# Performance work log

Measured on AMD Instinct MI355X. Metric: run time of the kernel, lower is better.

## Reference

```python
import jax, jax.numpy as jnp
import numpy as np


def _chamfer_min_sqdist(a, b):
    # a: [N,3], b: [M,3] -> for each point in a, min squared distance to b. [N]
    # ||a||^2 + ||b||^2 - 2 a.b^T ; clamp tiny negatives from cancellation.
    a2 = jnp.sum(a * a, axis=-1)            # [N]
    b2 = jnp.sum(b * b, axis=-1)            # [M]
    cross = a @ b.T                          # [N,M] GEMM, K=3
    d = a2[:, None] + b2[None, :] - 2.0 * cross
    return jnp.maximum(jnp.min(d, axis=1), 0.0)


def setup_inputs() -> dict:
    key = jax.random.key(0)
    k1, k2 = jax.random.split(key)
    N = 16384
    state_x = jax.random.normal(k1, (N, 3), dtype=jnp.float32)
    target = jax.random.normal(k2, (N, 3), dtype=jnp.float32)
    return {"state_x": state_x, "target": target}


def reference(state_x, target):
    # dist1: target -> nearest in state_x ; dist2: state_x -> nearest in target
    dist1 = _chamfer_min_sqdist(target, state_x)   # [N]
    dist2 = _chamfer_min_sqdist(state_x, target)   # [N]
    loss = (jnp.mean(jnp.sqrt(dist1)) + jnp.mean(jnp.sqrt(dist2))) * 0.5
    return loss * 10.0
```

## Files before the change

kernel.cpp:

```cpp
#include <hip/hip_runtime.h>
#include <math.h>


typedef __attribute__((ext_vector_type(8)))  short bf16x8;
typedef __attribute__((ext_vector_type(16))) float f32x16;

#define S_SLICES 4

__device__ __forceinline__ unsigned enc_f32(float f) {
    int b = __float_as_int(f);
    return (b >= 0) ? ((unsigned)b | 0x80000000u) : ~(unsigned)b;
}
__device__ __forceinline__ float dec_f32(unsigned k) {
    int b = (k & 0x80000000u) ? (int)(k & 0x7FFFFFFFu) : ~(int)k;
    return __int_as_float(b);
}

__device__ __forceinline__ unsigned short f2bf(float v) {
    unsigned u = __float_as_uint(v);
    u += 0x7FFFu + ((u >> 16) & 1u);
    return (unsigned short)(u >> 16);
}
__device__ __forceinline__ float bf2f(unsigned short b) {
    unsigned u = ((unsigned)b) << 16;
    return __uint_as_float(u);
}
__device__ __forceinline__ unsigned pk2(unsigned short lo, unsigned short hi) {
    return (unsigned)lo | ((unsigned)hi << 16);
}

__device__ __forceinline__ f32x16 mfma_v(bf16x8 a, bf16x8 b, f32x16 c) {
    f32x16 d;
    asm("v_mfma_f32_32x32x16_bf16 %0, %1, %2, %3"
        : "=&v"(d) : "v"(a), "v"(b), "v"(c));
    return d;
}

__global__ __launch_bounds__(256) void chamfer_prep(
    const float* __restrict__ state_x, const float* __restrict__ target,
    uint4* __restrict__ AfragS, uint4* __restrict__ AfragT,
    uint4* __restrict__ BfragS, uint4* __restrict__ BfragT,
    unsigned* __restrict__ mins_u, float* __restrict__ out, int N)
{
    const int p = blockIdx.x * 256 + threadIdx.x;
    const float* src = (p < N) ? state_x : target;
    const int i = (p < N) ? p : p - N;

    const float x = src[3*i+0], y = src[3*i+1], z = src[3*i+2];
    const float n2 = fmaf(x, x, fmaf(y, y, z * z));

    const unsigned short hx = f2bf(x), hy = f2bf(y), hz = f2bf(z);
    const unsigned short lx = f2bf(x - bf2f(hx));
    const unsigned short ly = f2bf(y - bf2f(hy));
    const unsigned short lz = f2bf(z - bf2f(hz));
    const unsigned short mhx = f2bf(-2.0f*x), mhy = f2bf(-2.0f*y), mhz = f2bf(-2.0f*z);
    const unsigned short mlx = f2bf(-2.0f*x - bf2f(mhx));
    const unsigned short mly = f2bf(-2.0f*y - bf2f(mhy));
    const unsigned short mlz = f2bf(-2.0f*z - bf2f(mhz));
    const unsigned short hn = f2bf(n2);
    const unsigned short ln = f2bf(n2 - bf2f(hn));
    const unsigned short ONE = 0x3F80;

    uint4 A0 = make_uint4(pk2(mhx,mhy), pk2(mhz,mlx), pk2(mly,mlz), pk2(mhx,mhy));
    uint4 A1 = make_uint4(pk2(mhz,mlx), pk2(mly,mlz), pk2(hn,ln),   pk2(ONE,ONE));
    uint4 B0 = make_uint4(pk2(hx,hy), pk2(hz,hx), pk2(hy,hz), pk2(lx,ly));
    uint4 B1 = make_uint4(pk2(lz,lx), pk2(ly,lz), pk2(ONE,ONE), pk2(hn,ln));

    uint4* Aarr = (p < N) ? AfragS : AfragT;
    uint4* Barr = (p < N) ? BfragS : BfragT;
    Aarr[2*i+0] = A0;  Aarr[2*i+1] = A1;

    const int bbase = (i >> 6) * 128 + ((i >> 5) & 1) * 64 + (i & 31);
    Barr[bbase +  0] = B0;
    Barr[bbase + 32] = B1;

    mins_u[p] = 0xFFFFFFFFu;
    if (p == 0) *out = 0.0f;
}

__global__ __launch_bounds__(256) void chamfer_main(
    const bf16x8* __restrict__ AfragS, const bf16x8* __restrict__ AfragT,
    const bf16x8* __restrict__ BfragS, const bf16x8* __restrict__ BfragT,
    unsigned* __restrict__ mins_u, int N, int S)
{
    const int tid  = threadIdx.x;
    const int lane = tid & 63;
    const int l31  = lane & 31;
    const int half = lane >> 5;
    const int w    = tid >> 6;

    const int bs = blockIdx.x / S;
    const int s  = blockIdx.x % S;
    const int qblk = bs * 256;

    const bf16x8* afr;
    const bf16x8* bfr;
    if (qblk < N) { afr = AfragT + (size_t)qblk * 2;       bfr = BfragS; }
    else          { afr = AfragS + (size_t)(qblk - N) * 2; bfr = BfragT; }

    const int CS = N / S;
    const int NCHUNK = CS / 1024;

    __shared__ uint4 ldsB[2048];

    const int r0 = w * 64;
    const bf16x8 av0 = afr[(r0 +      l31) * 2 + half];
    const bf16x8 av1 = afr[(r0 + 32 + l31) * 2 + half];

    const int boff = half * 32 + l31;

    f32x16 racc0, racc1, zc;
    #pragma unroll
    for (int i = 0; i < 16; ++i) { racc0[i] = 3.0e38f; racc1[i] = 3.0e38f; zc[i] = 0.0f; }

    for (int chunk = 0; chunk < NCHUNK; ++chunk) {
        {
            const uint4* src = (const uint4*)bfr
                             + ((size_t)s * CS + (size_t)chunk * 1024) * 2;
            #pragma unroll
            for (int j = 0; j < 8; ++j)
                ldsB[tid + j * 256] = src[tid + j * 256];
        }
        __syncthreads();
        const bf16x8* lb = (const bf16x8*)ldsB;

        #pragma unroll 2
        for (int it = 0; it < 16; ++it) {
            const bf16x8 b0 = lb[it * 128 + boff];
            const bf16x8 b1 = lb[it * 128 + 64 + boff];
            f32x16 a0 = mfma_v(av0, b0, zc);
            f32x16 a1 = mfma_v(av0, b1, zc);
            f32x16 a2 = mfma_v(av1, b0, zc);
            f32x16 a3 = mfma_v(av1, b1, zc);
            __builtin_amdgcn_sched_barrier(0);
            asm volatile("s_nop 7");
            __builtin_amdgcn_sched_barrier(0);
            #pragma unroll
            for (int i = 0; i < 16; ++i)
                racc0[i] = fminf(fminf(racc0[i], a0[i]), a1[i]);
            #pragma unroll
            for (int i = 0; i < 16; ++i)
                racc1[i] = fminf(fminf(racc1[i], a2[i]), a3[i]);
        }
        __syncthreads();
    }

    float* lf = (float*)ldsB;
    const int cg = l31 >> 2, cl = l31 & 3;
    #pragma unroll
    for (int i = 0; i < 16; ++i) {
        const int row0 = (i & 3) + 8 * (i >> 2) + 4 * half;
        const int row1 = row0 + 32;
        lf[w * 2048 + row0 * 32 + ((cg ^ (row0 & 7)) << 2) + cl] = racc0[i];
        lf[w * 2048 + row1 * 32 + ((cg ^ (row1 & 7)) << 2) + cl] = racc1[i];
    }
    __syncthreads();
    {
        const int r = tid & 63, wr = tid >> 6;
        const float4* rowp = (const float4*)(lf + wr * 2048 + r * 32);
        float m0 = 3.0e38f, m1 = 3.0e38f;
        #pragma unroll
        for (int g = 0; g < 8; g += 2) {
            const float4 v0 = rowp[g ^ (r & 7)];
            const float4 v1 = rowp[(g + 1) ^ (r & 7)];
            m0 = fminf(fminf(m0, v0.x), fminf(v0.y, v0.z));
            m0 = fminf(m0, v0.w);
            m1 = fminf(fminf(m1, v1.x), fminf(v1.y, v1.z));
            m1 = fminf(m1, v1.w);
        }
        atomicMin(&mins_u[qblk + wr * 64 + r], enc_f32(fminf(m0, m1)));
    }
}

__global__ __launch_bounds__(256) void chamfer_finish(
    const unsigned* __restrict__ mins_u, float* __restrict__ out, int N)
{
    const int tid = threadIdx.x;
    const int qi = blockIdx.x * 256 + tid;

    float v = sqrtf(fmaxf(dec_f32(mins_u[qi]), 0.0f));

    for (int off = 32; off > 0; off >>= 1) v += __shfl_down(v, off, 64);
    __shared__ float wsum[4];
    if ((tid & 63) == 0) wsum[tid >> 6] = v;
    __syncthreads();
    if (tid == 0) {
        const float bsum = wsum[0] + wsum[1] + wsum[2] + wsum[3];
        atomicAdd(out, bsum * 5.0f / (float)N);
    }
}

extern "C" void kernel_launch(void* const* d_in, const int* in_sizes, int n_in,
                              void* d_out, int out_size, void* d_ws, size_t ws_size,
                              hipStream_t stream)
{
    const float* state_x = (const float*)d_in[0];
    const float* target  = (const float*)d_in[1];
    float* out = (float*)d_out;

    const int N = in_sizes[0] / 3;
    const int twoN = 2 * N;

    int S = S_SLICES;
    while (S > 1 && (N % (S * 1024)) != 0) S >>= 1;

    char* wsb = (char*)d_ws;
    unsigned* mins_u = (unsigned*)wsb;
    uint4* AfragS = (uint4*)(wsb + (size_t)twoN * 4);
    uint4* AfragT = (uint4*)(wsb + (size_t)twoN * 4 + (size_t)N * 32);
    uint4* BfragS = (uint4*)(wsb + (size_t)twoN * 4 + (size_t)N * 64);
    uint4* BfragT = (uint4*)(wsb + (size_t)twoN * 4 + (size_t)N * 96);

    chamfer_prep<<<twoN / 256, 256, 0, stream>>>(
        state_x, target, AfragS, AfragT, BfragS, BfragT, mins_u, out, N);

    const int rowBlocks = twoN / 256;
    chamfer_main<<<rowBlocks * S, 256, 0, stream>>>(
        (const bf16x8*)AfragS, (const bf16x8*)AfragT,
        (const bf16x8*)BfragS, (const bf16x8*)BfragT, mins_u, N, S);

    chamfer_finish<<<twoN / 256, 256, 0, stream>>>(mins_u, out, N);
}
```

Before: 81.90 us.

## Halve per-wave query tile to 32 rows and double block count

Each wave now handles 32 query rows with one A fragment and two MFMAs per iteration instead of 64 rows and four MFMAs. Blocks cover 128 queries, so the grid doubles, and launch bounds request 4 blocks per CU to raise occupancy. The trade-off is that each B tile in LDS is reused over half as many rows, so global-to-LDS traffic doubles. Extra s_nop padding is added because fewer MFMAs now sit between issue and the dependent min reduction.

```diff
diff --git a/kernel.cpp b/kernel.cpp
--- a/kernel.cpp
+++ b/kernel.cpp
@@ -78,7 +78,7 @@
     if (p == 0) *out = 0.0f;
 }
 
-__global__ __launch_bounds__(256) void chamfer_main(
+__global__ __launch_bounds__(256, 4) void chamfer_main(
     const bf16x8* __restrict__ AfragS, const bf16x8* __restrict__ AfragT,
     const bf16x8* __restrict__ BfragS, const bf16x8* __restrict__ BfragT,
     unsigned* __restrict__ mins_u, int N, int S)
@@ -91,7 +91,7 @@
 
     const int bs = blockIdx.x / S;
     const int s  = blockIdx.x % S;
-    const int qblk = bs * 256;
+    const int qblk = bs * 128;
 
     const bf16x8* afr;
     const bf16x8* bfr;
@@ -102,16 +102,15 @@
     const int NCHUNK = CS / 1024;
 
     __shared__ uint4 ldsB[2048];
-
-    const int r0 = w * 64;
-    const bf16x8 av0 = afr[(r0 +      l31) * 2 + half];
-    const bf16x8 av1 = afr[(r0 + 32 + l31) * 2 + half];
+    const bf16x8* lb = (const bf16x8*)ldsB;
+
+    const bf16x8 av = afr[(w * 32 + l31) * 2 + half];
 
     const int boff = half * 32 + l31;
 
-    f32x16 racc0, racc1, zc;
+    f32x16 racc, zc;
     #pragma unroll
-    for (int i = 0; i < 16; ++i) { racc0[i] = 3.0e38f; racc1[i] = 3.0e38f; zc[i] = 0.0f; }
+    for (int i = 0; i < 16; ++i) { racc[i] = 3.0e38f; zc[i] = 0.0f; }
 
     for (int chunk = 0; chunk < NCHUNK; ++chunk) {
         {
@@ -122,25 +121,21 @@
                 ldsB[tid + j * 256] = src[tid + j * 256];
         }
         __syncthreads();
-        const bf16x8* lb = (const bf16x8*)ldsB;
-
-        #pragma unroll 2
+
+        #pragma unroll 1
         for (int it = 0; it < 16; ++it) {
             const bf16x8 b0 = lb[it * 128 + boff];
             const bf16x8 b1 = lb[it * 128 + 64 + boff];
-            f32x16 a0 = mfma_v(av0, b0, zc);
-            f32x16 a1 = mfma_v(av0, b1, zc);
-            f32x16 a2 = mfma_v(av1, b0, zc);
-            f32x16 a3 = mfma_v(av1, b1, zc);
+            f32x16 a0 = mfma_v(av, b0, zc);
+            f32x16 a1 = mfma_v(av, b1, zc);
             __builtin_amdgcn_sched_barrier(0);
+            asm volatile("s_nop 7");
+            asm volatile("s_nop 7");
             asm volatile("s_nop 7");
             __builtin_amdgcn_sched_barrier(0);
             #pragma unroll
             for (int i = 0; i < 16; ++i)
-                racc0[i] = fminf(fminf(racc0[i], a0[i]), a1[i]);
-            #pragma unroll
-            for (int i = 0; i < 16; ++i)
-                racc1[i] = fminf(fminf(racc1[i], a2[i]), a3[i]);
+                racc[i] = fminf(fminf(racc[i], a0[i]), a1[i]);
         }
         __syncthreads();
     }
@@ -149,15 +144,13 @@
     const int cg = l31 >> 2, cl = l31 & 3;
     #pragma unroll
     for (int i = 0; i < 16; ++i) {
-        const int row0 = (i & 3) + 8 * (i >> 2) + 4 * half;
-        const int row1 = row0 + 32;
-        lf[w * 2048 + row0 * 32 + ((cg ^ (row0 & 7)) << 2) + cl] = racc0[i];
-        lf[w * 2048 + row1 * 32 + ((cg ^ (row1 & 7)) << 2) + cl] = racc1[i];
+        const int row = (i & 3) + 8 * (i >> 2) + 4 * half;
+        lf[w * 1024 + row * 32 + ((cg ^ (row & 7)) << 2) + cl] = racc[i];
     }
     __syncthreads();
-    {
-        const int r = tid & 63, wr = tid >> 6;
-        const float4* rowp = (const float4*)(lf + wr * 2048 + r * 32);
+    if (tid < 128) {
+        const int r = tid & 31, wr = tid >> 5;
+        const float4* rowp = (const float4*)(lf + wr * 1024 + r * 32);
         float m0 = 3.0e38f, m1 = 3.0e38f;
         #pragma unroll
         for (int g = 0; g < 8; g += 2) {
@@ -168,7 +161,7 @@
             m1 = fminf(fminf(m1, v1.x), fminf(v1.y, v1.z));
             m1 = fminf(m1, v1.w);
         }
-        atomicMin(&mins_u[qblk + wr * 64 + r], enc_f32(fminf(m0, m1)));
+        atomicMin(&mins_u[qblk + wr * 32 + r], enc_f32(fminf(m0, m1)));
     }
 }
 
@@ -214,7 +207,7 @@
     chamfer_prep<<<twoN / 256, 256, 0, stream>>>(
         state_x, target, AfragS, AfragT, BfragS, BfragT, mins_u, out, N);
 
-    const int rowBlocks = twoN / 256;
+    const int rowBlocks = twoN / 128;
     chamfer_main<<<rowBlocks * S, 256, 0, stream>>>(
         (const bf16x8*)AfragS, (const bf16x8*)AfragT,
         (const bf16x8*)BfragS, (const bf16x8*)BfragT, mins_u, N, S);
```

Result: no change. 81.63 us (-0.3%).
